# Performance work log

Hardware: AMD Instinct MI355X
Metric: run time of the kernel (lower is better)

Reference implementation:

```python
import jax, jax.numpy as jnp
import numpy as np

B, T, V, DE, DD, DC = 64, 64, 32000, 512, 1024, 512


def setup_inputs() -> dict:
    key = jax.random.key(0)
    ks = jax.random.split(key, 8)
    s = lambda k, shape: jax.random.normal(k, shape, jnp.float32) * 0.02
    return {
        "context": jax.random.normal(ks[0], (B, DC), jnp.float32),
        "labels": jax.random.randint(ks[1], (B, T), 0, V),
        "emb": s(ks[2], (V, DE)),
        "W_ih": s(ks[3], (3 * DD, DE + DC)),
        "b_ih": jnp.zeros((3 * DD,), jnp.float32),
        "W_hh": s(ks[4], (3 * DD, DD)),
        "b_hh": jnp.zeros((3 * DD,), jnp.float32),
        "init": jnp.zeros((1, DD), jnp.float32),
        "W_out": s(ks[5], (V, DD)),
        "b_out": jnp.zeros((V,), jnp.float32),
        "bos_idx": 1,
    }


def _gru_cell(x, h, W_ih, b_ih, W_hh, b_hh):
    # PyTorch GRUCell: gates ordered (r, z, n)
    gi = x @ W_ih.T + b_ih
    gh = h @ W_hh.T + b_hh
    i_r, i_z, i_n = jnp.split(gi, 3, axis=-1)
    h_r, h_z, h_n = jnp.split(gh, 3, axis=-1)
    r = jax.nn.sigmoid(i_r + h_r)
    z = jax.nn.sigmoid(i_z + h_z)
    n = jnp.tanh(i_n + r * h_n)
    return (1.0 - z) * n + z * h


def reference(context, labels, emb, W_ih, b_ih, W_hh, b_hh, init, W_out, b_out, bos_idx):
    b, t = labels.shape
    # Teacher forcing: input token at step s is bos for s=0 else labels[:, s-1]
    tokens = jnp.concatenate(
        [jnp.full((b, 1), bos_idx, labels.dtype), labels[:, :-1]], axis=1
    )  # [b, t]
    words = emb[tokens]  # [b, t, d_emb]
    ctx = jnp.broadcast_to(context[:, None, :], (b, t, context.shape[-1]))
    x_seq = jnp.swapaxes(jnp.concatenate([words, ctx], axis=-1), 0, 1)  # [t, b, de+dc]

    h0 = jnp.broadcast_to(init, (b, init.shape[-1]))

    def step(h, x):
        h = _gru_cell(x, h, W_ih, b_ih, W_hh, b_hh)
        return h, h

    _, states = jax.lax.scan(step, h0, x_seq)  # [t, b, d_dec]
    logits = jnp.einsum("tbd,vd->btv", states, W_out) + b_out  # [b, t, vocab]
    return logits
```

## Files before the change

### kernel.cpp

```cpp
#include <hip/hip_runtime.h>

#define Bsz 64
#define Tsz 64
#define Vsz 32000
#define DEsz 512
#define DDsz 1024
#define DCsz 512
#define DIN 1024
#define G3 3072

typedef unsigned short u16;
typedef unsigned int   u32;
typedef unsigned long long u64;
typedef __attribute__((ext_vector_type(8))) __bf16 bf16x8;
typedef __attribute__((ext_vector_type(4))) float f32x4;

__device__ __forceinline__ u16 f2bf(float f) {
    union { float f; unsigned int u; } v; v.f = f;
    unsigned int r = v.u + 0x7fffu + ((v.u >> 16) & 1u);
    return (u16)(r >> 16);
}

__device__ __forceinline__ void gload_lds16(const u16* g, u16* l) {
    __builtin_amdgcn_global_load_lds(
        (const __attribute__((address_space(1))) void*)g,
        (__attribute__((address_space(3))) void*)l, 16, 0, 0);
}

__device__ __forceinline__ float fast_sigmoid(float x) {
    float xc = fminf(fmaxf(x, -30.f), 30.f);
    return 1.f / (1.f + __expf(-xc));
}
__device__ __forceinline__ float fast_tanh(float x) {
    float xc = fminf(fmaxf(x, -15.f), 15.f);
    float e = __expf(2.f * xc);
    return (e - 1.f) / (e + 1.f);
}

__global__ void f32_to_bf16(const float* __restrict__ src, u16* __restrict__ dst, long n) {
    long i = ((long)blockIdx.x * blockDim.x + threadIdx.x) * 4;
    if (i + 3 < n) {
        float4 v = *(const float4*)&src[i];
        dst[i + 0] = f2bf(v.x);
        dst[i + 1] = f2bf(v.y);
        dst[i + 2] = f2bf(v.z);
        dst[i + 3] = f2bf(v.w);
    }
}

__global__ void build_x(const float* __restrict__ emb, const float* __restrict__ ctx,
                        const int* __restrict__ labels, const int* __restrict__ bos,
                        u16* __restrict__ X) {
    int i = blockIdx.x;
    int b = i >> 6;
    int t = i & 63;
    int tok = (t == 0) ? *bos : labels[b * Tsz + (t - 1)];
    const float* s0 = emb + (long)tok * DEsz;
    const float* s1 = ctx + (long)b * DCsz;
    u16* dst = X + (long)i * DIN;
    for (int c = threadIdx.x; c < DEsz; c += blockDim.x) {
        dst[c]        = f2bf(s0[c]);
        dst[DEsz + c] = f2bf(s1[c]);
    }
}

__global__ __launch_bounds__(256) void gemm128(
    const u16* __restrict__ A, const u16* __restrict__ Bm,
    const float* __restrict__ bias, float* __restrict__ C,
    int N, int K, int mblk)
{
    __shared__ __align__(16) u16 As[128 * 32];
    __shared__ __align__(16) u16 Bs[128 * 32];
    __shared__ __align__(16) float stage[32 * 132];
    const int tid  = threadIdx.x;
    const int wave = tid >> 6;
    const int lane = tid & 63;
    const int wm = wave >> 1, wn = wave & 1;

    int nwg = gridDim.x;
    int wg  = blockIdx.x;
    int cpx = nwg >> 3;
    wg = (wg & 7) * cpx + (wg >> 3);
    const int bm = (wg % mblk) * 128;
    const int bn = (wg / mblk) * 128;

    const int sr = tid >> 2;
    const int sc = (tid & 3) * 8;
    const u16* ga0 = A  + (long)(bm + sr) * K + sc;
    const u16* ga1 = A  + (long)(bm + 64 + sr) * K + sc;
    const u16* gb0 = Bm + (long)(bn + sr) * K + sc;
    const u16* gb1 = Bm + (long)(bn + 64 + sr) * K + sc;
    u16* la0 = As + tid * 8;
    u16* la1 = As + 2048 + tid * 8;
    u16* lb0 = Bs + tid * 8;
    u16* lb1 = Bs + 2048 + tid * 8;

    const int fr = lane & 15;
    const int kh = (lane >> 4) * 8;

    f32x4 acc[4][4];
    #pragma unroll
    for (int i = 0; i < 4; ++i)
        #pragma unroll
        for (int j = 0; j < 4; ++j) acc[i][j] = f32x4{0.f, 0.f, 0.f, 0.f};

    for (int k0 = 0; k0 < K; k0 += 32) {
        gload_lds16(ga0 + k0, la0);
        gload_lds16(ga1 + k0, la1);
        gload_lds16(gb0 + k0, lb0);
        gload_lds16(gb1 + k0, lb1);
        __syncthreads();
        bf16x8 af[4], bf[4];
        #pragma unroll
        for (int mi = 0; mi < 4; ++mi)
            af[mi] = *(const bf16x8*)&As[(wm * 64 + mi * 16 + fr) * 32 + kh];
        #pragma unroll
        for (int ni = 0; ni < 4; ++ni)
            bf[ni] = *(const bf16x8*)&Bs[(wn * 64 + ni * 16 + fr) * 32 + kh];
        #pragma unroll
        for (int mi = 0; mi < 4; ++mi)
            #pragma unroll
            for (int ni = 0; ni < 4; ++ni)
                acc[mi][ni] = __builtin_amdgcn_mfma_f32_16x16x32_bf16(af[mi], bf[ni], acc[mi][ni], 0, 0, 0);
        __syncthreads();
    }

    const int r0 = (lane >> 4) * 4;
    float bv[4];
    #pragma unroll
    for (int ni = 0; ni < 4; ++ni) bv[ni] = bias[bn + wn * 64 + ni * 16 + fr];

    #pragma unroll
    for (int mi = 0; mi < 4; ++mi) {
        __syncthreads();
        #pragma unroll
        for (int ni = 0; ni < 4; ++ni) {
            int scol = wn * 64 + ni * 16 + fr;
            #pragma unroll
            for (int j = 0; j < 4; ++j)
                stage[(wm * 16 + r0 + j) * 132 + scol] = acc[mi][ni][j] + bv[ni];
        }
        __syncthreads();
        #pragma unroll
        for (int p = 0; p < 4; ++p) {
            int idx  = p * 256 + tid;
            int srow = idx >> 5;
            int sc4  = (idx & 31) * 4;
            f32x4 v = *(const f32x4*)&stage[srow * 132 + sc4];
            int grow = bm + mi * 16 + (srow & 15) + (srow >> 4) * 64;
            __builtin_nontemporal_store(v, (f32x4*)&C[(long)grow * N + bn + sc4]);
        }
    }
}

#define PF 16
__global__ __launch_bounds__(256) void gru_persist(
    const u16* __restrict__ Whh,
    const float* __restrict__ bhh,
    const float* __restrict__ gi,
    const float* __restrict__ initp,
    u16* __restrict__ hst,
    u16* __restrict__ hT,
    int* __restrict__ arr,
    int* __restrict__ rel)
{
    __builtin_amdgcn_fence(__ATOMIC_ACQUIRE, "agent");

    __shared__ __align__(16) u16 Wl[48 * 1032];
    __shared__ __align__(16) u16 h0l[1024];
    const int tid  = threadIdx.x;
    const int w    = tid >> 6;
    const int lane = tid & 63;
    const int c0   = blockIdx.x * 16;
    const int fr   = lane & 15;
    const int kh   = (lane >> 4) * 8;
    const int r0   = (lane >> 4) * 4;
    const int kb_s = blockIdx.x >> 1;
    const int kio  = (blockIdx.x & 1) * 16;

    for (int ch = tid; ch < 48 * 128; ch += 256) {
        int r  = ch >> 7;
        int cc = (ch & 127) * 8;
        int g  = r >> 4, i = r & 15;
        *(bf16x8*)&Wl[r * 1032 + cc] =
            *(const bf16x8*)&Whh[((long)g * DDsz + c0 + i) * DDsz + cc];
    }
    #pragma unroll
    for (int i = 0; i < 4; ++i) h0l[tid * 4 + i] = f2bf(initp[tid * 4 + i]);
    __syncthreads();

    float hc[4];
    { float v = initp[c0 + fr];
      #pragma unroll
      for (int j = 0; j < 4; ++j) hc[j] = v; }
    const float bR = bhh[c0 + fr];
    const float bZ = bhh[DDsz + c0 + fr];
    const float bN = bhh[2 * DDsz + c0 + fr];

    float gir[4], giz[4], gin_[4];
    #pragma unroll
    for (int j = 0; j < 4; ++j) {
        long gib = ((long)(w * 16 + r0 + j) * Tsz) * G3 + c0 + fr;
        gir[j]  = gi[gib];
        giz[j]  = gi[gib + DDsz];
        gin_[j] = gi[gib + 2 * DDsz];
    }

    for (int t = 0; t < Tsz; ++t) {
        f32x4 acc[3];
        #pragma unroll
        for (int g = 0; g < 3; ++g) acc[g] = f32x4{0.f, 0.f, 0.f, 0.f};

        auto mfma3 = [&](bf16x8 a, int k) {
            bf16x8 wr_ = *(const bf16x8*)&Wl[(0  + fr) * 1032 + k * 32 + kh];
            bf16x8 wz_ = *(const bf16x8*)&Wl[(16 + fr) * 1032 + k * 32 + kh];
            bf16x8 wn_ = *(const bf16x8*)&Wl[(32 + fr) * 1032 + k * 32 + kh];
            acc[0] = __builtin_amdgcn_mfma_f32_16x16x32_bf16(a, wr_, acc[0], 0, 0, 0);
            acc[1] = __builtin_amdgcn_mfma_f32_16x16x32_bf16(a, wz_, acc[1], 0, 0, 0);
            acc[2] = __builtin_amdgcn_mfma_f32_16x16x32_bf16(a, wn_, acc[2], 0, 0, 0);
        };

        if (t == 0) {
            #pragma unroll
            for (int k = 0; k < 32; ++k) mfma3(*(const bf16x8*)&h0l[k * 32 + kh], k);
        } else {
            const u16* q0 = hT + ((long)(t - 1) * 32 * 64 + w * 16) * 32 + fr * 32 + kh;
            bf16x8 p0[PF];
            #pragma unroll
            for (int p = 0; p < PF; ++p) p0[p] = *(const bf16x8*)(q0 + p * 2048);
            #pragma unroll
            for (int k = 0; k < 32; ++k) {
                bf16x8 a = p0[k & (PF - 1)];
                if (k < 32 - PF) p0[k & (PF - 1)] = *(const bf16x8*)(q0 + (k + PF) * 2048);
                mfma3(a, k);
            }
        }

        #pragma unroll
        for (int j = 0; j < 4; ++j) {
            int b = w * 16 + r0 + j;
            float r = fast_sigmoid(gir[j] + acc[0][j] + bR);
            float z = fast_sigmoid(giz[j] + acc[1][j] + bZ);
            float n = fast_tanh(gin_[j] + r * (acc[2][j] + bN));
            float h = (1.f - z) * n + z * hc[j];
            hc[j] = h;
            int hb = (int)f2bf(h);
            int pb = __shfl_xor(hb, 1, 64);
            if (!(fr & 1)) {
                u32 val = ((u32)pb << 16) | (u32)hb;
                __hip_atomic_store(
                    (u32*)(hT + (((long)t * 32 + kb_s) * 64 + b) * 32 + kio + fr), val,
                    __ATOMIC_RELAXED, __HIP_MEMORY_SCOPE_AGENT);
                __builtin_nontemporal_store(
                    val, (u32*)(hst + ((long)b * Tsz + t) * DDsz + c0 + fr));
            }
        }

        if (t != Tsz - 1) {
            asm volatile("" ::: "memory");

            int tp = t + 1;
            #pragma unroll
            for (int j = 0; j < 4; ++j) {
                long gib = ((long)(w * 16 + r0 + j) * Tsz + tp) * G3 + c0 + fr;
                gir[j]  = gi[gib];
                giz[j]  = gi[gib + DDsz];
                gin_[j] = gi[gib + 2 * DDsz];
            }

            asm volatile("s_waitcnt vmcnt(12)" ::: "memory");
            __builtin_amdgcn_s_barrier();
            if (tid == 0) {
                __hip_atomic_fetch_add(&arr[(blockIdx.x & 7) << 4], 1,
                                       __ATOMIC_RELAXED, __HIP_MEMORY_SCOPE_AGENT);
                if (blockIdx.x == 0) {
                    const int tgt = 64 * (t + 1);
                    for (;;) {
                        int s = 0;
                        #pragma unroll
                        for (int g = 0; g < 8; ++g)
                            s += __hip_atomic_load(&arr[g << 4], __ATOMIC_RELAXED,
                                                   __HIP_MEMORY_SCOPE_AGENT);
                        if (s >= tgt) break;
                    }
                    #pragma unroll
                    for (int g = 0; g < 8; ++g)
                        __hip_atomic_store(&rel[g << 4], t + 1,
                                           __ATOMIC_RELAXED, __HIP_MEMORY_SCOPE_AGENT);
                } else {
                    while (__hip_atomic_load(&rel[(blockIdx.x & 7) << 4],
                                             __ATOMIC_RELAXED,
                                             __HIP_MEMORY_SCOPE_AGENT) < t + 1) { }
                }
            }
            __syncthreads();
        }
    }
}

extern "C" void kernel_launch(void* const* d_in, const int* in_sizes, int n_in,
                              void* d_out, int out_size, void* d_ws, size_t ws_size,
                              hipStream_t stream) {
    const float* ctx    = (const float*)d_in[0];
    const int*   labels = (const int*)  d_in[1];
    const float* emb    = (const float*)d_in[2];
    const float* W_ih   = (const float*)d_in[3];
    const float* b_ih   = (const float*)d_in[4];
    const float* W_hh   = (const float*)d_in[5];
    const float* b_hh   = (const float*)d_in[6];
    const float* initp  = (const float*)d_in[7];
    const float* W_out  = (const float*)d_in[8];
    const float* b_out  = (const float*)d_in[9];
    const int*   bos    = (const int*)  d_in[10];
    float* out = (float*)d_out;

    char* ws = (char*)d_ws;
    u16*   Xbf    = (u16*)  (ws + 0L);
    float* gi     = (float*)(ws + 8388608L);
    u16*   hst    = (u16*)  (ws + 58720256L);
    u16*   hT     = (u16*)  (ws + 67108864L);
    u16*   Wih_b  = (u16*)  (ws + 75497472L);
    u16*   Whh_b  = (u16*)  (ws + 81788928L);
    u16*   Wout_b = (u16*)  (ws + 88080384L);
    int*   arr    = (int*)  (ws + 153616384L);
    int*   rel    = (int*)  (ws + 153617408L);

    (void)hipMemsetAsync(arr, 0, 2048, stream);

    long n1 = (long)G3 * DIN;
    long n2 = (long)Vsz * DDsz;
    f32_to_bf16<<<(unsigned)(n1 / 4 / 256), 256, 0, stream>>>(W_ih, Wih_b, n1);
    f32_to_bf16<<<(unsigned)(n1 / 4 / 256), 256, 0, stream>>>(W_hh, Whh_b, n1);
    f32_to_bf16<<<(unsigned)(n2 / 4 / 256), 256, 0, stream>>>(W_out, Wout_b, n2);

    build_x<<<Bsz * Tsz, 128, 0, stream>>>(emb, ctx, labels, bos, Xbf);

    gemm128<<<(4096 / 128) * (G3 / 128), 256, 0, stream>>>(
        Xbf, Wih_b, b_ih, gi, G3, DIN, 4096 / 128);

    gru_persist<<<DDsz / 16, 256, 0, stream>>>(Whh_b, b_hh, gi, initp,
                                               hst, hT, arr, rel);

    gemm128<<<(4096 / 128) * (Vsz / 128), 256, 0, stream>>>(
        hst, Wout_b, b_out, out, Vsz, DDsz, 4096 / 128);
}
```

Measured before the change: 936.7 us.

## Fuse GRU recurrence with output projection GEMM in one cooperative kernel

Launches a single cooperative kernel of 256 blocks. 64 blocks run the persistent GRU recurrence, and the other 192 blocks compute the vocabulary projection tiles as soon as each pair of timesteps (128 rows of time-major hidden states) is released via the rel flags. The goal is to overlap the large output GEMM with the latency-bound recurrence on idle CUs. To support this, hidden states are stored time-major with a permuted output row mapping and the prefetch depth is reduced to 8. Risks include consumers polling the shared rel flags, memory bandwidth contention slowing the recurrence, and losing the separate tuned GEMM's occupancy.

```diff
diff --git a/kernel.cpp b/kernel.cpp
--- a/kernel.cpp
+++ b/kernel.cpp
@@ -8,6 +8,9 @@
 #define DCsz 512
 #define DIN 1024
 #define G3 3072
+#define NCONS 192
+#define NTT 250
+#define NMT 32
 
 typedef unsigned short u16;
 typedef unsigned int   u32;
@@ -153,122 +156,127 @@
     }
 }
 
-#define PF 16
-__global__ __launch_bounds__(256) void gru_persist(
-    const u16* __restrict__ Whh,
-    const float* __restrict__ bhh,
-    const float* __restrict__ gi,
-    const float* __restrict__ initp,
+#define PF 8
+__global__ __launch_bounds__(256) void fused(
+    const u16* __restrict__ Whh, const float* __restrict__ bhh,
+    const float* __restrict__ gi, const float* __restrict__ initp,
     u16* __restrict__ hst,
     u16* __restrict__ hT,
-    int* __restrict__ arr,
-    int* __restrict__ rel)
+    int* __restrict__ arr, int* __restrict__ rel,
+    const u16* __restrict__ Wout, const float* __restrict__ bout,
+    float* __restrict__ out)
 {
     __builtin_amdgcn_fence(__ATOMIC_ACQUIRE, "agent");
 
-    __shared__ __align__(16) u16 Wl[48 * 1032];
-    __shared__ __align__(16) u16 h0l[1024];
-    const int tid  = threadIdx.x;
-    const int w    = tid >> 6;
-    const int lane = tid & 63;
-    const int c0   = blockIdx.x * 16;
-    const int fr   = lane & 15;
-    const int kh   = (lane >> 4) * 8;
-    const int r0   = (lane >> 4) * 4;
-    const int kb_s = blockIdx.x >> 1;
-    const int kio  = (blockIdx.x & 1) * 16;
-
-    for (int ch = tid; ch < 48 * 128; ch += 256) {
-        int r  = ch >> 7;
-        int cc = (ch & 127) * 8;
-        int g  = r >> 4, i = r & 15;
-        *(bf16x8*)&Wl[r * 1032 + cc] =
-            *(const bf16x8*)&Whh[((long)g * DDsz + c0 + i) * DDsz + cc];
-    }
-    #pragma unroll
-    for (int i = 0; i < 4; ++i) h0l[tid * 4 + i] = f2bf(initp[tid * 4 + i]);
-    __syncthreads();
-
-    float hc[4];
-    { float v = initp[c0 + fr];
-      #pragma unroll
-      for (int j = 0; j < 4; ++j) hc[j] = v; }
-    const float bR = bhh[c0 + fr];
-    const float bZ = bhh[DDsz + c0 + fr];
-    const float bN = bhh[2 * DDsz + c0 + fr];
-
-    float gir[4], giz[4], gin_[4];
-    #pragma unroll
-    for (int j = 0; j < 4; ++j) {
-        long gib = ((long)(w * 16 + r0 + j) * Tsz) * G3 + c0 + fr;
-        gir[j]  = gi[gib];
-        giz[j]  = gi[gib + DDsz];
-        gin_[j] = gi[gib + 2 * DDsz];
-    }
-
-    for (int t = 0; t < Tsz; ++t) {
-        f32x4 acc[3];
-        #pragma unroll
-        for (int g = 0; g < 3; ++g) acc[g] = f32x4{0.f, 0.f, 0.f, 0.f};
-
-        auto mfma3 = [&](bf16x8 a, int k) {
-            bf16x8 wr_ = *(const bf16x8*)&Wl[(0  + fr) * 1032 + k * 32 + kh];
-            bf16x8 wz_ = *(const bf16x8*)&Wl[(16 + fr) * 1032 + k * 32 + kh];
-            bf16x8 wn_ = *(const bf16x8*)&Wl[(32 + fr) * 1032 + k * 32 + kh];
-            acc[0] = __builtin_amdgcn_mfma_f32_16x16x32_bf16(a, wr_, acc[0], 0, 0, 0);
-            acc[1] = __builtin_amdgcn_mfma_f32_16x16x32_bf16(a, wz_, acc[1], 0, 0, 0);
-            acc[2] = __builtin_amdgcn_mfma_f32_16x16x32_bf16(a, wn_, acc[2], 0, 0, 0);
-        };
-
-        if (t == 0) {
-            #pragma unroll
-            for (int k = 0; k < 32; ++k) mfma3(*(const bf16x8*)&h0l[k * 32 + kh], k);
-        } else {
-            const u16* q0 = hT + ((long)(t - 1) * 32 * 64 + w * 16) * 32 + fr * 32 + kh;
-            bf16x8 p0[PF];
-            #pragma unroll
-            for (int p = 0; p < PF; ++p) p0[p] = *(const bf16x8*)(q0 + p * 2048);
-            #pragma unroll
-            for (int k = 0; k < 32; ++k) {
-                bf16x8 a = p0[k & (PF - 1)];
-                if (k < 32 - PF) p0[k & (PF - 1)] = *(const bf16x8*)(q0 + (k + PF) * 2048);
-                mfma3(a, k);
-            }
-        }
-
+    __shared__ __align__(16) char smem[101376];
+    const int tid = threadIdx.x;
+
+    if (blockIdx.x < 64) {
+        u16* Wl  = (u16*)smem;
+        u16* h0l = (u16*)(smem + 99072 * 2 - 99072);
+        h0l = (u16*)(smem + 99072);
+        const int w    = tid >> 6;
+        const int lane = tid & 63;
+        const int c0   = blockIdx.x * 16;
+        const int fr   = lane & 15;
+        const int kh   = (lane >> 4) * 8;
+        const int r0   = (lane >> 4) * 4;
+        const int kb_s = blockIdx.x >> 1;
+        const int kio  = (blockIdx.x & 1) * 16;
+
+        for (int ch = tid; ch < 48 * 128; ch += 256) {
+            int r  = ch >> 7;
+            int cc = (ch & 127) * 8;
+            int g  = r >> 4, i = r & 15;
+            *(bf16x8*)&Wl[r * 1032 + cc] =
+                *(const bf16x8*)&Whh[((long)g * DDsz + c0 + i) * DDsz + cc];
+        }
+        #pragma unroll
+        for (int i = 0; i < 4; ++i) h0l[tid * 4 + i] = f2bf(initp[tid * 4 + i]);
+        __syncthreads();
+
+        float hc[4];
+        { float v = initp[c0 + fr];
+          #pragma unroll
+          for (int j = 0; j < 4; ++j) hc[j] = v; }
+        const float bR = bhh[c0 + fr];
+        const float bZ = bhh[DDsz + c0 + fr];
+        const float bN = bhh[2 * DDsz + c0 + fr];
+
+        float gir[4], giz[4], gin_[4];
         #pragma unroll
         for (int j = 0; j < 4; ++j) {
-            int b = w * 16 + r0 + j;
-            float r = fast_sigmoid(gir[j] + acc[0][j] + bR);
-            float z = fast_sigmoid(giz[j] + acc[1][j] + bZ);
-            float n = fast_tanh(gin_[j] + r * (acc[2][j] + bN));
-            float h = (1.f - z) * n + z * hc[j];
-            hc[j] = h;
-            int hb = (int)f2bf(h);
-            int pb = __shfl_xor(hb, 1, 64);
-            if (!(fr & 1)) {
-                u32 val = ((u32)pb << 16) | (u32)hb;
-                __hip_atomic_store(
-                    (u32*)(hT + (((long)t * 32 + kb_s) * 64 + b) * 32 + kio + fr), val,
-                    __ATOMIC_RELAXED, __HIP_MEMORY_SCOPE_AGENT);
-                __builtin_nontemporal_store(
-                    val, (u32*)(hst + ((long)b * Tsz + t) * DDsz + c0 + fr));
-            }
-        }
-
-        if (t != Tsz - 1) {
+            long gib = ((long)(w * 16 + r0 + j) * Tsz) * G3 + c0 + fr;
+            gir[j]  = gi[gib];
+            giz[j]  = gi[gib + DDsz];
+            gin_[j] = gi[gib + 2 * DDsz];
+        }
+
+        for (int t = 0; t < Tsz; ++t) {
+            f32x4 acc[3];
+            #pragma unroll
+            for (int g = 0; g < 3; ++g) acc[g] = f32x4{0.f, 0.f, 0.f, 0.f};
+
+            auto mfma3 = [&](bf16x8 a, int k) {
+                bf16x8 wr_ = *(const bf16x8*)&Wl[(0  + fr) * 1032 + k * 32 + kh];
+                bf16x8 wz_ = *(const bf16x8*)&Wl[(16 + fr) * 1032 + k * 32 + kh];
+                bf16x8 wn_ = *(const bf16x8*)&Wl[(32 + fr) * 1032 + k * 32 + kh];
+                acc[0] = __builtin_amdgcn_mfma_f32_16x16x32_bf16(a, wr_, acc[0], 0, 0, 0);
+                acc[1] = __builtin_amdgcn_mfma_f32_16x16x32_bf16(a, wz_, acc[1], 0, 0, 0);
+                acc[2] = __builtin_amdgcn_mfma_f32_16x16x32_bf16(a, wn_, acc[2], 0, 0, 0);
+            };
+
+            if (t == 0) {
+                #pragma unroll
+                for (int k = 0; k < 32; ++k) mfma3(*(const bf16x8*)&h0l[k * 32 + kh], k);
+            } else {
+                const u16* q0 = hT + ((long)(t - 1) * 32 * 64 + w * 16) * 32 + fr * 32 + kh;
+                bf16x8 p0[PF];
+                #pragma unroll
+                for (int p = 0; p < PF; ++p) p0[p] = *(const bf16x8*)(q0 + p * 2048);
+                #pragma unroll
+                for (int k = 0; k < 32; ++k) {
+                    bf16x8 a = p0[k & (PF - 1)];
+                    if (k < 32 - PF) p0[k & (PF - 1)] = *(const bf16x8*)(q0 + (k + PF) * 2048);
+                    mfma3(a, k);
+                }
+            }
+
+            #pragma unroll
+            for (int j = 0; j < 4; ++j) {
+                int b = w * 16 + r0 + j;
+                float r = fast_sigmoid(gir[j] + acc[0][j] + bR);
+                float z = fast_sigmoid(giz[j] + acc[1][j] + bZ);
+                float n = fast_tanh(gin_[j] + r * (acc[2][j] + bN));
+                float h = (1.f - z) * n + z * hc[j];
+                hc[j] = h;
+                int hb = (int)f2bf(h);
+                int pb = __shfl_xor(hb, 1, 64);
+                if (!(fr & 1)) {
+                    u32 val = ((u32)pb << 16) | (u32)hb;
+                    __hip_atomic_store(
+                        (u32*)(hT + (((long)t * 32 + kb_s) * 64 + b) * 32 + kio + fr), val,
+                        __ATOMIC_RELAXED, __HIP_MEMORY_SCOPE_AGENT);
+                    __hip_atomic_store(
+                        (u32*)(hst + ((long)t * Bsz + b) * DDsz + c0 + fr), val,
+                        __ATOMIC_RELAXED, __HIP_MEMORY_SCOPE_AGENT);
+                }
+            }
+
             asm volatile("" ::: "memory");
-
-            int tp = t + 1;
-            #pragma unroll
-            for (int j = 0; j < 4; ++j) {
-                long gib = ((long)(w * 16 + r0 + j) * Tsz + tp) * G3 + c0 + fr;
-                gir[j]  = gi[gib];
-                giz[j]  = gi[gib + DDsz];
-                gin_[j] = gi[gib + 2 * DDsz];
-            }
-
-            asm volatile("s_waitcnt vmcnt(12)" ::: "memory");
+            if (t != Tsz - 1) {
+                int tp = t + 1;
+                #pragma unroll
+                for (int j = 0; j < 4; ++j) {
+                    long gib = ((long)(w * 16 + r0 + j) * Tsz + tp) * G3 + c0 + fr;
+                    gir[j]  = gi[gib];
+                    giz[j]  = gi[gib + DDsz];
+                    gin_[j] = gi[gib + 2 * DDsz];
+                }
+                asm volatile("s_waitcnt vmcnt(12)" ::: "memory");
+            } else {
+                asm volatile("s_waitcnt vmcnt(0)" ::: "memory");
+            }
             __builtin_amdgcn_s_barrier();
             if (tid == 0) {
                 __hip_atomic_fetch_add(&arr[(blockIdx.x & 7) << 4], 1,
@@ -295,6 +303,98 @@
             }
             __syncthreads();
         }
+    } else {
+        u16*   As    = (u16*)smem;
+        u16*   Bs    = (u16*)(smem + 8192);
+        float* stage = (float*)(smem + 16384);
+        const int cid  = blockIdx.x - 64;
+        const int wave = tid >> 6;
+        const int lane = tid & 63;
+        const int wm = wave >> 1, wn = wave & 1;
+        const int sr = tid >> 2;
+        const int sc = (tid & 3) * 8;
+        const int fr = lane & 15;
+        const int kh = (lane >> 4) * 8;
+        const int r0 = (lane >> 4) * 4;
+        u16* la0 = As + tid * 8;
+        u16* la1 = As + 2048 + tid * 8;
+        u16* lb0 = Bs + tid * 8;
+        u16* lb1 = Bs + 2048 + tid * 8;
+
+        int lastmt = -1;
+        for (int j = cid; j < NMT * NTT; j += NCONS) {
+            int mt = j / NTT;
+            int nt = j - mt * NTT;
+            if (mt != lastmt) {
+                if (tid == 0) {
+                    while (__hip_atomic_load(&rel[(cid & 7) << 4], __ATOMIC_RELAXED,
+                                             __HIP_MEMORY_SCOPE_AGENT) < 2 * mt + 2)
+                        __builtin_amdgcn_s_sleep(8);
+                }
+                __syncthreads();
+                lastmt = mt;
+            }
+            const int bm = mt * 128;
+            const int bn = nt * 128;
+            const u16* ga0 = hst  + (long)(bm + sr) * DDsz + sc;
+            const u16* ga1 = hst  + (long)(bm + 64 + sr) * DDsz + sc;
+            const u16* gb0 = Wout + (long)(bn + sr) * DDsz + sc;
+            const u16* gb1 = Wout + (long)(bn + 64 + sr) * DDsz + sc;
+
+            f32x4 acc[4][4];
+            #pragma unroll
+            for (int i = 0; i < 4; ++i)
+                #pragma unroll
+                for (int jj = 0; jj < 4; ++jj) acc[i][jj] = f32x4{0.f, 0.f, 0.f, 0.f};
+
+            for (int k0 = 0; k0 < DDsz; k0 += 32) {
+                gload_lds16(ga0 + k0, la0);
+                gload_lds16(ga1 + k0, la1);
+                gload_lds16(gb0 + k0, lb0);
+                gload_lds16(gb1 + k0, lb1);
+                __syncthreads();
+                bf16x8 af[4], bf[4];
+                #pragma unroll
+                for (int mi = 0; mi < 4; ++mi)
+                    af[mi] = *(const bf16x8*)&As[(wm * 64 + mi * 16 + fr) * 32 + kh];
+                #pragma unroll
+                for (int ni = 0; ni < 4; ++ni)
+                    bf[ni] = *(const bf16x8*)&Bs[(wn * 64 + ni * 16 + fr) * 32 + kh];
+                #pragma unroll
+                for (int mi = 0; mi < 4; ++mi)
+                    #pragma unroll
+                    for (int ni = 0; ni < 4; ++ni)
+                        acc[mi][ni] = __builtin_amdgcn_mfma_f32_16x16x32_bf16(af[mi], bf[ni], acc[mi][ni], 0, 0, 0);
+                __syncthreads();
+            }
+
+            float bv[4];
+            #pragma unroll
+            for (int ni = 0; ni < 4; ++ni) bv[ni] = bout[bn + wn * 64 + ni * 16 + fr];
+
+            #pragma unroll
+            for (int mi = 0; mi < 4; ++mi) {
+                __syncthreads();
+                #pragma unroll
+                for (int ni = 0; ni < 4; ++ni) {
+                    int scol = wn * 64 + ni * 16 + fr;
+                    #pragma unroll
+                    for (int jj = 0; jj < 4; ++jj)
+                        stage[(wm * 16 + r0 + jj) * 132 + scol] = acc[mi][ni][jj] + bv[ni];
+                }
+                __syncthreads();
+                #pragma unroll
+                for (int p = 0; p < 4; ++p) {
+                    int idx  = p * 256 + tid;
+                    int srow = idx >> 5;
+                    int sc4  = (idx & 31) * 4;
+                    f32x4 v = *(const f32x4*)&stage[srow * 132 + sc4];
+                    int r = bm + mi * 16 + (srow & 15) + (srow >> 4) * 64;
+                    int orow = ((r & 63) << 6) | (r >> 6);
+                    __builtin_nontemporal_store(v, (f32x4*)&out[(long)orow * Vsz + bn + sc4]);
+                }
+            }
+        }
     }
 }
 
@@ -338,9 +438,16 @@
     gemm128<<<(4096 / 128) * (G3 / 128), 256, 0, stream>>>(
         Xbf, Wih_b, b_ih, gi, G3, DIN, 4096 / 128);
 
-    gru_persist<<<DDsz / 16, 256, 0, stream>>>(Whh_b, b_hh, gi, initp,
-                                               hst, hT, arr, rel);
-
-    gemm128<<<(4096 / 128) * (Vsz / 128), 256, 0, stream>>>(
-        hst, Wout_b, b_out, out, Vsz, DDsz, 4096 / 128);
-}
+    {
+        const u16* Whh_c = Whh_b; const float* bhh_c = b_hh;
+        const float* gi_c = gi;   const float* init_c = initp;
+        u16* hst_c = hst;         u16* hT_c = hT;
+        int* arr_c = arr;         int* rel_c = rel;
+        const u16* Wout_c = Wout_b; const float* bout_c = b_out;
+        float* out_c = out;
+        void* kargs[] = {&Whh_c, &bhh_c, &gi_c, &init_c, &hst_c, &hT_c,
+                         &arr_c, &rel_c, &Wout_c, &bout_c, &out_c};
+        (void)hipLaunchCooperativeKernel((const void*)fused, dim3(256), dim3(256),
+                                         kargs, 0, stream);
+    }
+}
```

Result: slower. 957.6 us (+2.2%).

## Split GRU grid barrier into per-batch-chain wave-level syncs and read hT in output GEMM

Applied to the files above, without the earlier changes.

The persistent GRU kernel drops its block-wide __syncthreads barrier. Each wave now signals its own counter line, and two independent chains (batch halves, wave pairs) are released separately, so one half of the batch can advance without waiting for the other. The duplicate hst state store is removed, and a new output GEMM reads hidden states directly from the transposed hT buffer and remaps output rows, saving a write stream inside the recurrent loop. PF also shrinks from 16 to 8. The risks are correctness of the cross-wave dependencies now that the intra-block barrier is gone, and less coalesced A loads in the new GEMM.

```diff
diff --git a/kernel.cpp b/kernel.cpp
--- a/kernel.cpp
+++ b/kernel.cpp
@@ -153,13 +153,103 @@
     }
 }
 
-#define PF 16
+__global__ __launch_bounds__(256) void gemm_hT(
+    const u16* __restrict__ hT, const u16* __restrict__ Bm,
+    const float* __restrict__ bias, float* __restrict__ C,
+    int N, int mblk)
+{
+    __shared__ __align__(16) u16 As[128 * 32];
+    __shared__ __align__(16) u16 Bs[128 * 32];
+    __shared__ __align__(16) float stage[32 * 132];
+    const int tid  = threadIdx.x;
+    const int wave = tid >> 6;
+    const int lane = tid & 63;
+    const int wm = wave >> 1, wn = wave & 1;
+
+    int nwg = gridDim.x;
+    int wg  = blockIdx.x;
+    int cpx = nwg >> 3;
+    wg = (wg & 7) * cpx + (wg >> 3);
+    const int bm = (wg % mblk) * 128;
+    const int bn = (wg / mblk) * 128;
+
+    const int sr = tid >> 2;
+    const int sc = (tid & 3) * 8;
+    const int rA0 = bm + sr, rA1 = bm + 64 + sr;
+    const u16* ga0 = hT + (long)(rA0 >> 6) * 65536 + (rA0 & 63) * 32 + sc;
+    const u16* ga1 = hT + (long)(rA1 >> 6) * 65536 + (rA1 & 63) * 32 + sc;
+    const u16* gb0 = Bm + (long)(bn + sr) * DDsz + sc;
+    const u16* gb1 = Bm + (long)(bn + 64 + sr) * DDsz + sc;
+    u16* la0 = As + tid * 8;
+    u16* la1 = As + 2048 + tid * 8;
+    u16* lb0 = Bs + tid * 8;
+    u16* lb1 = Bs + 2048 + tid * 8;
+
+    const int fr = lane & 15;
+    const int kh = (lane >> 4) * 8;
+
+    f32x4 acc[4][4];
+    #pragma unroll
+    for (int i = 0; i < 4; ++i)
+        #pragma unroll
+        for (int j = 0; j < 4; ++j) acc[i][j] = f32x4{0.f, 0.f, 0.f, 0.f};
+
+    for (int k0 = 0; k0 < DDsz; k0 += 32) {
+        gload_lds16(ga0 + k0 * 64, la0);
+        gload_lds16(ga1 + k0 * 64, la1);
+        gload_lds16(gb0 + k0, lb0);
+        gload_lds16(gb1 + k0, lb1);
+        __syncthreads();
+        bf16x8 af[4], bf[4];
+        #pragma unroll
+        for (int mi = 0; mi < 4; ++mi)
+            af[mi] = *(const bf16x8*)&As[(wm * 64 + mi * 16 + fr) * 32 + kh];
+        #pragma unroll
+        for (int ni = 0; ni < 4; ++ni)
+            bf[ni] = *(const bf16x8*)&Bs[(wn * 64 + ni * 16 + fr) * 32 + kh];
+        #pragma unroll
+        for (int mi = 0; mi < 4; ++mi)
+            #pragma unroll
+            for (int ni = 0; ni < 4; ++ni)
+                acc[mi][ni] = __builtin_amdgcn_mfma_f32_16x16x32_bf16(af[mi], bf[ni], acc[mi][ni], 0, 0, 0);
+        __syncthreads();
+    }
+
+    const int r0 = (lane >> 4) * 4;
+    float bv[4];
+    #pragma unroll
+    for (int ni = 0; ni < 4; ++ni) bv[ni] = bias[bn + wn * 64 + ni * 16 + fr];
+
+    #pragma unroll
+    for (int mi = 0; mi < 4; ++mi) {
+        __syncthreads();
+        #pragma unroll
+        for (int ni = 0; ni < 4; ++ni) {
+            int scol = wn * 64 + ni * 16 + fr;
+            #pragma unroll
+            for (int j = 0; j < 4; ++j)
+                stage[(wm * 16 + r0 + j) * 132 + scol] = acc[mi][ni][j] + bv[ni];
+        }
+        __syncthreads();
+        #pragma unroll
+        for (int p = 0; p < 4; ++p) {
+            int idx  = p * 256 + tid;
+            int srow = idx >> 5;
+            int sc4  = (idx & 31) * 4;
+            f32x4 v = *(const f32x4*)&stage[srow * 132 + sc4];
+            int r    = bm + mi * 16 + (srow & 15) + (srow >> 4) * 64;
+            int orow = ((r & 63) << 6) | (r >> 6);
+            __builtin_nontemporal_store(v, (f32x4*)&C[(long)orow * N + bn + sc4]);
+        }
+    }
+}
+
+#define PF 8
 __global__ __launch_bounds__(256) void gru_persist(
     const u16* __restrict__ Whh,
     const float* __restrict__ bhh,
     const float* __restrict__ gi,
     const float* __restrict__ initp,
-    u16* __restrict__ hst,
     u16* __restrict__ hT,
     int* __restrict__ arr,
     int* __restrict__ rel)
@@ -177,6 +267,8 @@
     const int r0   = (lane >> 4) * 4;
     const int kb_s = blockIdx.x >> 1;
     const int kio  = (blockIdx.x & 1) * 16;
+    const int chain  = w >> 1;
+    const int myline = ((chain << 3) | (blockIdx.x & 7)) << 4;
 
     for (int ch = tid; ch < 48 * 128; ch += 256) {
         int r  = ch >> 7;
@@ -251,8 +343,6 @@
                 __hip_atomic_store(
                     (u32*)(hT + (((long)t * 32 + kb_s) * 64 + b) * 32 + kio + fr), val,
                     __ATOMIC_RELAXED, __HIP_MEMORY_SCOPE_AGENT);
-                __builtin_nontemporal_store(
-                    val, (u32*)(hst + ((long)b * Tsz + t) * DDsz + c0 + fr));
             }
         }
 
@@ -269,31 +359,29 @@
             }
 
             asm volatile("s_waitcnt vmcnt(12)" ::: "memory");
-            __builtin_amdgcn_s_barrier();
-            if (tid == 0) {
-                __hip_atomic_fetch_add(&arr[(blockIdx.x & 7) << 4], 1,
+
+            if (lane == 0) {
+                __hip_atomic_fetch_add(&arr[myline], 1,
                                        __ATOMIC_RELAXED, __HIP_MEMORY_SCOPE_AGENT);
-                if (blockIdx.x == 0) {
-                    const int tgt = 64 * (t + 1);
+                if (blockIdx.x == 0 && (w & 1) == 0) {
+                    const int tgt = 128 * (t + 1);
                     for (;;) {
                         int s = 0;
                         #pragma unroll
                         for (int g = 0; g < 8; ++g)
-                            s += __hip_atomic_load(&arr[g << 4], __ATOMIC_RELAXED,
+                            s += __hip_atomic_load(&arr[((chain << 3) | g) << 4],
+                                                   __ATOMIC_RELAXED,
                                                    __HIP_MEMORY_SCOPE_AGENT);
                         if (s >= tgt) break;
                     }
-                    #pragma unroll
-                    for (int g = 0; g < 8; ++g)
-                        __hip_atomic_store(&rel[g << 4], t + 1,
-                                           __ATOMIC_RELAXED, __HIP_MEMORY_SCOPE_AGENT);
+                    __hip_atomic_store(&rel[chain << 4], t + 1,
+                                       __ATOMIC_RELAXED, __HIP_MEMORY_SCOPE_AGENT);
                 } else {
-                    while (__hip_atomic_load(&rel[(blockIdx.x & 7) << 4],
-                                             __ATOMIC_RELAXED,
+                    while (__hip_atomic_load(&rel[chain << 4], __ATOMIC_RELAXED,
                                              __HIP_MEMORY_SCOPE_AGENT) < t + 1) { }
                 }
             }
-            __syncthreads();
+            asm volatile("" ::: "memory");
         }
     }
 }
@@ -317,7 +405,6 @@
     char* ws = (char*)d_ws;
     u16*   Xbf    = (u16*)  (ws + 0L);
     float* gi     = (float*)(ws + 8388608L);
-    u16*   hst    = (u16*)  (ws + 58720256L);
     u16*   hT     = (u16*)  (ws + 67108864L);
     u16*   Wih_b  = (u16*)  (ws + 75497472L);
     u16*   Whh_b  = (u16*)  (ws + 81788928L);
@@ -338,9 +425,8 @@
     gemm128<<<(4096 / 128) * (G3 / 128), 256, 0, stream>>>(
         Xbf, Wih_b, b_ih, gi, G3, DIN, 4096 / 128);
 
-    gru_persist<<<DDsz / 16, 256, 0, stream>>>(Whh_b, b_hh, gi, initp,
-                                               hst, hT, arr, rel);
-
-    gemm128<<<(4096 / 128) * (Vsz / 128), 256, 0, stream>>>(
-        hst, Wout_b, b_out, out, Vsz, DDsz, 4096 / 128);
-}
+    gru_persist<<<DDsz / 16, 256, 0, stream>>>(Whh_b, b_hh, gi, initp, hT, arr, rel);
+
+    gemm_hT<<<(4096 / 128) * (Vsz / 128), 256, 0, stream>>>(
+        hT, Wout_b, b_out, out, Vsz, 4096 / 128);
+}
```

New measurement: 877.7 us. 1.07x faster.
